# Kernel optimization log

Measured on AMD Instinct MI355X. Metric: run time of the kernel, lower is better.

The kernel has to match this reference:

```python
import jax, jax.numpy as jnp
import numpy as np

B, C, H, W = 4, 64, 64, 64
C8 = C // 8


def cl_attention(x, gamma):
    # DANet CAM-style channel attention: [B,C,H,W] -> [B,C,H,W]
    b, c, h, w = x.shape
    xf = x.reshape(b, c, h * w)                       # b c n
    energy = jnp.einsum('bcn,bdn->bcd', xf, xf)       # b c c
    energy = jnp.max(energy, axis=-1, keepdims=True) - energy
    attn = jax.nn.softmax(energy, axis=-1)
    out = jnp.einsum('bcd,bdn->bcn', attn, xf).reshape(b, c, h, w)
    return gamma * out + x


def setup_inputs() -> dict:
    key = jax.random.key(0)
    ks = jax.random.split(key, 8)
    s = 0.02
    return {
        'cnn_feat': jax.random.normal(ks[0], (B, C, H, W), jnp.float32),
        'vit_feat': jax.random.normal(ks[1], (B, C, H, W), jnp.float32),
        'Wq': jax.random.normal(ks[2], (C8, C), jnp.float32) * s,   # 1x1 conv kernel
        'bq': jnp.zeros((C8,), jnp.float32),
        'Wk': jax.random.normal(ks[3], (C8, C), jnp.float32) * s,
        'bk': jnp.zeros((C8,), jnp.float32),
        'Wv': jax.random.normal(ks[4], (C, C), jnp.float32) * s,
        'bv': jnp.zeros((C,), jnp.float32),
        'gamma': jnp.zeros((1,), jnp.float32),
        'gamma_cla_cnn': jnp.zeros((1,), jnp.float32),
        'gamma_cla_vit': jnp.zeros((1,), jnp.float32),
    }


def reference(cnn_feat, vit_feat, Wq, bq, Wk, bk, Wv, bv, gamma,
              gamma_cla_cnn, gamma_cla_vit):
    b, c, h, w = cnn_feat.shape
    n = h * w

    cnn_att = cl_attention(cnn_feat, gamma_cla_cnn)   # b c h w
    vit_att = cl_attention(vit_feat, gamma_cla_vit)   # b c h w

    # query: 1x1 conv -> view(b, C8, n) -> permute -> (b, n, C8)
    q = jnp.einsum('bchw,oc->bhwo', cnn_att, Wq).reshape(b, n, -1) + bq

    # vit: rearrange 'b c h w -> b (h w) c'
    vit_flat = vit_att.reshape(b, c, n).transpose(0, 2, 1)          # b n c
    k = vit_flat @ Wk.T + bk                                        # b n C8
    v = vit_flat @ Wv.T + bv                                        # b n C

    energy = jnp.einsum('bqd,bkd->bqk', q, k)                       # b n n
    attn = jax.nn.softmax(energy, axis=-1)
    out = jnp.einsum('bqk,bkc->bqc', attn, v)                       # b n c
    out = out.transpose(0, 2, 1).reshape(b, c, h, w)                # 'b (h w) c -> b c h w'
    return gamma * out + cnn_feat
```

## Files before the change

### kernel.cpp

```cpp
#include <hip/hip_runtime.h>
#include <hip/hip_bf16.h>

#define BSZ 4
#define CC 64
#define NN 4096
#define CN (CC*NN)
#define BCN (BSZ*CN)

typedef __attribute__((ext_vector_type(4))) float    f4v;
typedef __attribute__((ext_vector_type(4))) int      i4v;
typedef __attribute__((ext_vector_type(2))) int      i2v;
typedef __attribute__((ext_vector_type(8))) short    s8v;

__device__ __forceinline__ unsigned pack_bf16(float lo, float hi) {
    unsigned l = __builtin_bit_cast(unsigned, lo);
    unsigned h = __builtin_bit_cast(unsigned, hi);
    return (h & 0xFFFF0000u) | (l >> 16);
}
__device__ __forceinline__ unsigned pack2(float lo, float hi) {
    float2 f2; f2.x = lo; f2.y = hi;
    __hip_bfloat162 h = __float22bfloat162_rn(f2);
    unsigned u;
    __builtin_memcpy(&u, &h, 4);
    return u;
}

__global__ __launch_bounds__(256) void gram_k(const float* __restrict__ cnn,
                                              const float* __restrict__ vit,
                                              float* __restrict__ part) {
    __shared__ __align__(16) float sXT[128*68];
    int t = threadIdx.x;
    int blk = blockIdx.x;
    int ch = blk & 31, b = (blk >> 5) & 3, i2 = blk >> 7;
    const float* X = (i2 ? vit : cnn) + b * CN;
    int n0 = ch * 128;
#pragma unroll
    for (int j = 0; j < 8; j++) {
        int idx = t + j * 256;
        int c = idx >> 5, n4 = idx & 31;
        f4v val = *(const f4v*)&X[c * NN + n0 + n4 * 4];
        int base = (n4 * 4) * 68 + c;
        sXT[base]       = val[0];
        sXT[base + 68]  = val[1];
        sXT[base + 136] = val[2];
        sXT[base + 204] = val[3];
    }
    __syncthreads();
    int tc = (t & 15) * 4, td = (t >> 4) * 4;
    f4v acc[4];
#pragma unroll
    for (int i = 0; i < 4; i++) acc[i] = (f4v){0.f, 0.f, 0.f, 0.f};
#pragma unroll 4
    for (int k = 0; k < 128; k++) {
        f4v a  = *(const f4v*)&sXT[k * 68 + tc];
        f4v bb = *(const f4v*)&sXT[k * 68 + td];
#pragma unroll
        for (int i = 0; i < 4; i++) acc[i] += a[i] * bb;
    }
    float* dst = part + ch * 32768 + (i2 * 4 + b) * 4096;
#pragma unroll
    for (int i = 0; i < 4; i++) *(f4v*)&dst[(tc + i) * 64 + td] = acc[i];
}

__global__ void gred_k(const float* __restrict__ part, float* __restrict__ G) {
    int row = blockIdx.x;
    int d = threadIdx.x;
    float s = 0.f;
#pragma unroll 8
    for (int ch = 0; ch < 32; ch++) s += part[ch * 32768 + row * 64 + d];
    float mn = s;
#pragma unroll
    for (int off = 1; off < 64; off <<= 1) mn = fminf(mn, __shfl_xor(mn, off));
    float e = __expf(mn - s);
    float sm = e;
#pragma unroll
    for (int off = 1; off < 64; off <<= 1) sm += __shfl_xor(sm, off);
    G[row * 64 + d] = e / sm;
}

__global__ __launch_bounds__(256) void qkvw_k(const float* __restrict__ cnn,
                                              const float* __restrict__ vit,
                                              const float* __restrict__ G,
                                              const float* __restrict__ Wq,
                                              const float* __restrict__ Wk,
                                              const float* __restrict__ Wv,
                                              const float* __restrict__ gcnn,
                                              const float* __restrict__ gvit,
                                              const float* __restrict__ bq,
                                              const float* __restrict__ bk,
                                              const float* __restrict__ bv,
                                              ushort* __restrict__ qb,
                                              ushort* __restrict__ kb,
                                              ushort* __restrict__ vF) {
    __shared__ __align__(16) float sA[8192];
    __shared__ float sWt[5200];
    int t = threadIdx.x;
    int b = blockIdx.x >> 6, ktg = blockIdx.x & 63, n0 = ktg * 64;
    int w = t >> 6, lane = t & 63, c15 = lane & 15, q4 = lane >> 4;
    int n = n0 + w * 16 + c15;
    const float LOG2E = 1.44269504f;

#pragma unroll
    for (int i = 0; i < 4; i++) {
        int idx = (i * 256 + t) * 4;
        *(f4v*)&sA[idx]        = *(const f4v*)&G[(size_t)b * 4096 + idx];
        *(f4v*)&sA[4096 + idx] = *(const f4v*)&G[(size_t)(4 + b) * 4096 + idx];
    }
    __syncthreads();

    {
        int r16 = w, c = t & 63;
        float gc = *gcnn, gv = *gvit;
        float acc[4][5];
#pragma unroll
        for (int mi = 0; mi < 4; mi++)
#pragma unroll
            for (int tl = 0; tl < 5; tl++) acc[mi][tl] = 0.f;
#pragma unroll 4
        for (int d = 0; d < 64; d++) {
            float av = sA[4096 + d * 64 + c];
            float ac = sA[d * 64 + c];
#pragma unroll
            for (int mi = 0; mi < 4; mi++) {
                int m = mi * 4 + r16;
                if (mi < 2)
                    acc[mi][0] += Wq[m * 64 + d] * ac;
                else
                    acc[mi][0] += Wk[(m - 8) * 64 + d] * av;
#pragma unroll
                for (int tl = 1; tl < 5; tl++)
                    acc[mi][tl] += Wv[((tl - 1) * 16 + m) * 64 + d] * av;
            }
        }
#pragma unroll
        for (int mi = 0; mi < 4; mi++) {
            int m = mi * 4 + r16;
            if (mi < 2)
                sWt[m * 65 + c] = gc * acc[mi][0] + Wq[m * 64 + c];
            else
                sWt[m * 65 + c] = gv * acc[mi][0] + Wk[(m - 8) * 64 + c];
#pragma unroll
            for (int tl = 1; tl < 5; tl++)
                sWt[tl * 1040 + m * 65 + c] =
                    gv * acc[mi][tl] + Wv[((tl - 1) * 16 + m) * 64 + c];
        }
    }
    __syncthreads();

    s8v A[10];
#pragma unroll
    for (int i = 0; i < 10; i++) {
        int tile = i >> 1, frag = i & 1;
        const float* src = &sWt[tile * 1040 + (lane & 15) * 65 + frag * 32 + q4 * 8];
        i4v o;
#pragma unroll
        for (int p = 0; p < 4; p++)
            o[p] = (int)pack_bf16(src[2 * p], src[2 * p + 1]);
        A[i] = __builtin_bit_cast(s8v, o);
    }

    s8v Bc[2], Bv[2];
#pragma unroll
    for (int f = 0; f < 2; f++) {
        i4v pc, pv;
#pragma unroll
        for (int p = 0; p < 4; p++) {
            int c0 = f * 32 + q4 * 8 + p * 2;
            size_t a0 = (size_t)b * CN + (size_t)c0 * NN + n;
            pc[p] = (int)pack_bf16(cnn[a0], cnn[a0 + NN]);
            pv[p] = (int)pack_bf16(vit[a0], vit[a0 + NN]);
        }
        Bc[f] = __builtin_bit_cast(s8v, pc);
        Bv[f] = __builtin_bit_cast(s8v, pv);
    }

    f4v acc = *(const f4v*)(bq + (q4 & 1) * 4);
    acc = __builtin_amdgcn_mfma_f32_16x16x32_bf16(A[0], Bc[0], acc, 0, 0, 0);
    acc = __builtin_amdgcn_mfma_f32_16x16x32_bf16(A[1], Bc[1], acc, 0, 0, 0);
    if (q4 < 2) {
        unsigned d0 = pack_bf16(acc[0] * LOG2E, acc[1] * LOG2E);
        unsigned d1 = pack_bf16(acc[2] * LOG2E, acc[3] * LOG2E);
        unsigned long long v = ((unsigned long long)d1 << 32) | d0;
        *(unsigned long long*)&qb[(size_t)(b * NN + n) * 8 + q4 * 4] = v;
    }
    acc = *(const f4v*)(bk + (q4 & 1) * 4);
    acc = __builtin_amdgcn_mfma_f32_16x16x32_bf16(A[0], Bv[0], acc, 0, 0, 0);
    acc = __builtin_amdgcn_mfma_f32_16x16x32_bf16(A[1], Bv[1], acc, 0, 0, 0);
    if (q4 >= 2) {
        unsigned d0 = pack_bf16(acc[0], acc[1]), d1 = pack_bf16(acc[2], acc[3]);
        unsigned long long v = ((unsigned long long)d1 << 32) | d0;
        *(unsigned long long*)&kb[(size_t)(b * NN + n) * 8 + (q4 - 2) * 4] = v;
    }
    float* vbuf = sA;
#pragma unroll
    for (int tile = 1; tile < 5; tile++) {
        acc = *(const f4v*)(bv + (tile - 1) * 16 + q4 * 4);
        acc = __builtin_amdgcn_mfma_f32_16x16x32_bf16(A[tile * 2],     Bv[0], acc, 0, 0, 0);
        acc = __builtin_amdgcn_mfma_f32_16x16x32_bf16(A[tile * 2 + 1], Bv[1], acc, 0, 0, 0);
#pragma unroll
        for (int r = 0; r < 4; r++)
            vbuf[((tile - 1) * 16 + q4 * 4 + r) * 67 + w * 16 + c15] = acc[r];
    }
    __syncthreads();
    {
        int nt = w;
#pragma unroll
        for (int F = 0; F < 2; F++) {
            float vv[8];
#pragma unroll
            for (int e = 0; e < 8; e++)
                vv[e] = vbuf[(nt * 16 + c15) * 67 + 32 * F + 16 * (e >> 2)
                             + 4 * q4 + (e & 3)];
            i4v o;
#pragma unroll
            for (int p = 0; p < 4; p++)
                o[p] = (int)pack_bf16(vv[2 * p], vv[2 * p + 1]);
            *(i4v*)&vF[((size_t)((b * 64 + ktg) * 8 + nt * 2 + F)) * 512 + lane * 8] = o;
        }
    }
}

__global__ __launch_bounds__(256, 2) void flashB(
        const ushort* __restrict__ qb, const ushort* __restrict__ kb,
        const ushort* __restrict__ vF, const float* __restrict__ cnn,
        const float* __restrict__ gamma, float* __restrict__ out) {
    __shared__ __align__(16) float sO[2][64 * 68];
    __shared__ float sL[4][64];
    __shared__ float sRv[64];

    int t = threadIdx.x;
    int lane = t & 63, w = t >> 6;
    int c15 = lane & 15, q4 = lane >> 4;
    int blk = blockIdx.x;
    int b = blk >> 6, q0 = (blk & 63) * 64;
    float gm = *gamma;

    s8v qB[4];
#pragma unroll
    for (int g = 0; g < 4; g++) {
        i4v qa = (i4v){0, 0, 0, 0};
        if (q4 == 0)
            qa = *(const i4v*)(qb + (size_t)(b * NN + q0 + g * 16 + c15) * 8);
        qB[g] = __builtin_bit_cast(s8v, qa);
    }

    f4v accO[4][4];
#pragma unroll
    for (int g = 0; g < 4; g++)
#pragma unroll
        for (int nt = 0; nt < 4; nt++) accO[g][nt] = (f4v){0.f, 0.f, 0.f, 0.f};
    float lacc[4] = {0.f, 0.f, 0.f, 0.f};

    const ushort* kbb = kb + (size_t)b * NN * 8 + (size_t)c15 * 8;
    const ushort* vfb = vF + (size_t)b * 64 * 8 * 512 + (size_t)lane * 8;
    int kq = w * 1024;

    i4v bkc[4];
#pragma unroll
    for (int nt = 0; nt < 4; nt++)
        bkc[nt] = *(const i4v*)(kbb + (size_t)(kq + nt * 16) * 8);

    for (int kt = 0; kt < 16; kt++) {
        int ktg = (kq >> 6) + kt;
        i4v vA[2][4];
#pragma unroll
        for (int F = 0; F < 2; F++)
#pragma unroll
            for (int nt = 0; nt < 4; nt++)
                vA[F][nt] = *(const i4v*)(vfb +
                    (size_t)(ktg * 8 + nt * 2 + F) * 512);
        i4v bkn[4];
        if (kt < 15) {
#pragma unroll
            for (int nt = 0; nt < 4; nt++)
                bkn[nt] = *(const i4v*)(kbb +
                    (size_t)(kq + (kt + 1) * 64 + nt * 16) * 8);
        }

#pragma unroll
        for (int g = 0; g < 4; g++) {
            f4v z = (f4v){0.f, 0.f, 0.f, 0.f};
            f4v S[4];
#pragma unroll
            for (int nt = 0; nt < 4; nt++)
                S[nt] = __builtin_amdgcn_mfma_f32_16x16x32_bf16(
                    __builtin_bit_cast(s8v, bkc[nt]), qB[g], z, 0, 0, 0);
            f4v p[4];
            float ps = 0.f;
#pragma unroll
            for (int nt = 0; nt < 4; nt++)
#pragma unroll
                for (int rr = 0; rr < 4; rr++) {
                    p[nt][rr] = __builtin_amdgcn_exp2f(S[nt][rr]);
                    ps += p[nt][rr];
                }
            lacc[g] += ps;
            s8v Bp[2];
#pragma unroll
            for (int F = 0; F < 2; F++) {
                i4v bp;
                bp[0] = (int)pack2(p[2 * F][0],     p[2 * F][1]);
                bp[1] = (int)pack2(p[2 * F][2],     p[2 * F][3]);
                bp[2] = (int)pack2(p[2 * F + 1][0], p[2 * F + 1][1]);
                bp[3] = (int)pack2(p[2 * F + 1][2], p[2 * F + 1][3]);
                Bp[F] = __builtin_bit_cast(s8v, bp);
            }
            __builtin_amdgcn_s_setprio(1);
#pragma unroll
            for (int F = 0; F < 2; F++)
#pragma unroll
                for (int nt = 0; nt < 4; nt++)
                    accO[g][nt] = __builtin_amdgcn_mfma_f32_16x16x32_bf16(
                        __builtin_bit_cast(s8v, vA[F][nt]), Bp[F],
                        accO[g][nt], 0, 0, 0);
            __builtin_amdgcn_s_setprio(0);
        }
        if (kt < 15) {
#pragma unroll
            for (int nt = 0; nt < 4; nt++) bkc[nt] = bkn[nt];
        }
    }

#pragma unroll
    for (int g = 0; g < 4; g++) {
        lacc[g] += __shfl_xor(lacc[g], 16);
        lacc[g] += __shfl_xor(lacc[g], 32);
        if (q4 == 0) sL[w][g * 16 + c15] = lacc[g];
    }
    if (w >= 2) {
        float* s = sO[w - 2];
#pragma unroll
        for (int g = 0; g < 4; g++)
#pragma unroll
            for (int nt = 0; nt < 4; nt++)
#pragma unroll
                for (int rr = 0; rr < 4; rr++)
                    s[(nt * 16 + q4 * 4 + rr) * 68 + g * 16 + c15] = accO[g][nt][rr];
    }
    __syncthreads();
    if (w < 2) {
        float* s = sO[w];
#pragma unroll
        for (int g = 0; g < 4; g++)
#pragma unroll
            for (int nt = 0; nt < 4; nt++)
#pragma unroll
                for (int rr = 0; rr < 4; rr++)
                    accO[g][nt][rr] += s[(nt * 16 + q4 * 4 + rr) * 68 + g * 16 + c15];
    }
    if (w == 1) {
        float* s = sO[1];
#pragma unroll
        for (int g = 0; g < 4; g++)
#pragma unroll
            for (int nt = 0; nt < 4; nt++)
#pragma unroll
                for (int rr = 0; rr < 4; rr++)
                    s[(nt * 16 + q4 * 4 + rr) * 68 + g * 16 + c15] = accO[g][nt][rr];
    }
    if (w == 2) {
        float Ls = sL[0][lane] + sL[1][lane] + sL[2][lane] + sL[3][lane];
        sRv[lane] = gm / Ls;
    }
    __syncthreads();
    if (w == 0) {
        float* s1 = sO[1];
        float* s0 = sO[0];
#pragma unroll
        for (int g = 0; g < 4; g++)
#pragma unroll
            for (int nt = 0; nt < 4; nt++)
#pragma unroll
                for (int rr = 0; rr < 4; rr++) {
                    int off = (nt * 16 + q4 * 4 + rr) * 68 + g * 16 + c15;
                    s0[off] = accO[g][nt][rr] + s1[off];
                }
    }
    __syncthreads();
#pragma unroll
    for (int it = 0; it < 4; it++) {
        int c = it * 16 + (t >> 4), l16 = t & 15, q = l16 * 4;
        f4v o  = *(const f4v*)&sO[0][c * 68 + q];
        f4v rv = *(const f4v*)&sRv[q];
        size_t gi = (size_t)(b * 64 + c) * NN + q0 + q;
        f4v cv = *(const f4v*)&cnn[gi];
        *(f4v*)&out[gi] = o * rv + cv;
    }
}

extern "C" void kernel_launch(void* const* d_in, const int* in_sizes, int n_in,
                              void* d_out, int out_size, void* d_ws, size_t ws_size,
                              hipStream_t stream) {
    const float* cnn  = (const float*)d_in[0];
    const float* vit  = (const float*)d_in[1];
    const float* Wq   = (const float*)d_in[2];
    const float* bq   = (const float*)d_in[3];
    const float* Wk   = (const float*)d_in[4];
    const float* bk   = (const float*)d_in[5];
    const float* Wv   = (const float*)d_in[6];
    const float* bv   = (const float*)d_in[7];
    const float* gam  = (const float*)d_in[8];
    const float* gcnn = (const float*)d_in[9];
    const float* gvit = (const float*)d_in[10];
    float* out = (float*)d_out;

    float* ws = (float*)d_ws;
    float*  part = ws;
    float*  G    = ws + 1048576;
    ushort* qb   = (ushort*)(ws + 1081344);
    ushort* kb   = (ushort*)(ws + 1146880);
    ushort* vF   = (ushort*)(ws + 1212416);

    gram_k<<<256, 256, 0, stream>>>(cnn, vit, part);
    gred_k<<<512, 64,  0, stream>>>(part, G);
    qkvw_k<<<256, 256, 0, stream>>>(cnn, vit, G, Wq, Wk, Wv, gcnn, gvit,
                                    bq, bk, bv, qb, kb, vF);
    flashB<<<256, 256, 0, stream>>>(qb, kb, vF, cnn, gam, out);
}
```

Before: 123.0 us.

## Split flash attention keys across eight waves and coalesce gram partial layout

The flash kernel now runs 512 threads per block, so eight waves each handle 512 keys instead of four waves handling 1024. A tree reduction of the partial outputs through four shared-memory buffers replaces the old two-buffer scheme. The gram kernel stages its 64x64 partial tile through shared memory and writes it contiguously per chunk, and the reduction kernel reads it with vector loads and shuffles. The aim is more latency hiding and coalesced partial traffic, at the cost of more shared memory, extra barriers and possible occupancy limits at 512 threads.

Result: no change. 121.5 us (-1.2%).

```diff
diff --git a/kernel.cpp b/kernel.cpp
--- a/kernel.cpp
+++ b/kernel.cpp
@@ -57,25 +57,53 @@
 #pragma unroll
         for (int i = 0; i < 4; i++) acc[i] += a[i] * bb;
     }
-    float* dst = part + ch * 32768 + (i2 * 4 + b) * 4096;
-#pragma unroll
-    for (int i = 0; i < 4; i++) *(f4v*)&dst[(tc + i) * 64 + td] = acc[i];
+    __syncthreads();
+    float* sOut = sXT;
+#pragma unroll
+    for (int i = 0; i < 4; i++)
+        *(f4v*)&sOut[(tc + i) * 65 + td] = acc[i];
+    __syncthreads();
+    float* dst = part + (size_t)((i2 * 4 + b) * 32 + ch) * 4096;
+#pragma unroll
+    for (int j = 0; j < 4; j++) {
+        int flat = j * 1024 + t * 4;
+        int r = flat >> 6, d = flat & 63;
+        *(f4v*)&dst[flat] = *(const f4v*)&sOut[r * 65 + d];
+    }
 }
 
 __global__ void gred_k(const float* __restrict__ part, float* __restrict__ G) {
-    int row = blockIdx.x;
-    int d = threadIdx.x;
-    float s = 0.f;
-#pragma unroll 8
-    for (int ch = 0; ch < 32; ch++) s += part[ch * 32768 + row * 64 + d];
-    float mn = s;
-#pragma unroll
-    for (int off = 1; off < 64; off <<= 1) mn = fminf(mn, __shfl_xor(mn, off));
-    float e = __expf(mn - s);
-    float sm = e;
-#pragma unroll
-    for (int off = 1; off < 64; off <<= 1) sm += __shfl_xor(sm, off);
-    G[row * 64 + d] = e / sm;
+    int R = blockIdx.x;
+    int t = threadIdx.x;
+    int i2b = R >> 6, r = R & 63;
+    int l16 = t & 15, grp = t >> 4;
+    const float* base = part + (size_t)i2b * 32 * 4096 + r * 64 + l16 * 4;
+    f4v s = (f4v){0.f, 0.f, 0.f, 0.f};
+#pragma unroll
+    for (int c8 = 0; c8 < 8; c8++)
+        s += *(const f4v*)(base + (size_t)(c8 * 4 + grp) * 4096);
+#pragma unroll
+    for (int off = 16; off < 64; off <<= 1) {
+        s[0] += __shfl_xor(s[0], off);
+        s[1] += __shfl_xor(s[1], off);
+        s[2] += __shfl_xor(s[2], off);
+        s[3] += __shfl_xor(s[3], off);
+    }
+    float mn = fminf(fminf(s[0], s[1]), fminf(s[2], s[3]));
+#pragma unroll
+    for (int off = 1; off < 16; off <<= 1) mn = fminf(mn, __shfl_xor(mn, off));
+    f4v e;
+    float sm = 0.f;
+#pragma unroll
+    for (int j = 0; j < 4; j++) { e[j] = __expf(mn - s[j]); sm += e[j]; }
+#pragma unroll
+    for (int off = 1; off < 16; off <<= 1) sm += __shfl_xor(sm, off);
+    if (t < 16) {
+        f4v o;
+#pragma unroll
+        for (int j = 0; j < 4; j++) o[j] = e[j] / sm;
+        *(f4v*)&G[(size_t)R * 64 + l16 * 4] = o;
+    }
 }
 
 __global__ __launch_bounds__(256) void qkvw_k(const float* __restrict__ cnn,
@@ -220,13 +248,13 @@
     }
 }
 
-__global__ __launch_bounds__(256, 2) void flashB(
+__global__ __launch_bounds__(512, 2) void flashB(
         const ushort* __restrict__ qb, const ushort* __restrict__ kb,
         const ushort* __restrict__ vF, const float* __restrict__ cnn,
         const float* __restrict__ gamma, float* __restrict__ out) {
-    __shared__ __align__(16) float sO[2][64 * 68];
-    __shared__ float sL[4][64];
-    __shared__ float sRv[64];
+    __shared__ __align__(16) float sO[4][64 * 68];
+    __shared__ float sL[8][64];
+    __shared__ __align__(16) float sRv[64];
 
     int t = threadIdx.x;
     int lane = t & 63, w = t >> 6;
@@ -253,14 +281,14 @@
 
     const ushort* kbb = kb + (size_t)b * NN * 8 + (size_t)c15 * 8;
     const ushort* vfb = vF + (size_t)b * 64 * 8 * 512 + (size_t)lane * 8;
-    int kq = w * 1024;
+    int kq = w * 512;
 
     i4v bkc[4];
 #pragma unroll
     for (int nt = 0; nt < 4; nt++)
         bkc[nt] = *(const i4v*)(kbb + (size_t)(kq + nt * 16) * 8);
 
-    for (int kt = 0; kt < 16; kt++) {
+    for (int kt = 0; kt < 8; kt++) {
         int ktg = (kq >> 6) + kt;
         i4v vA[2][4];
 #pragma unroll
@@ -270,7 +298,7 @@
                 vA[F][nt] = *(const i4v*)(vfb +
                     (size_t)(ktg * 8 + nt * 2 + F) * 512);
         i4v bkn[4];
-        if (kt < 15) {
+        if (kt < 7) {
 #pragma unroll
             for (int nt = 0; nt < 4; nt++)
                 bkn[nt] = *(const i4v*)(kbb +
@@ -315,7 +343,7 @@
                         accO[g][nt], 0, 0, 0);
             __builtin_amdgcn_s_setprio(0);
         }
-        if (kt < 15) {
+        if (kt < 7) {
 #pragma unroll
             for (int nt = 0; nt < 4; nt++) bkc[nt] = bkn[nt];
         }
@@ -327,8 +355,8 @@
         lacc[g] += __shfl_xor(lacc[g], 32);
         if (q4 == 0) sL[w][g * 16 + c15] = lacc[g];
     }
-    if (w >= 2) {
-        float* s = sO[w - 2];
+
+    auto WRS = [&](float* s) {
 #pragma unroll
         for (int g = 0; g < 4; g++)
 #pragma unroll
@@ -336,10 +364,8 @@
 #pragma unroll
                 for (int rr = 0; rr < 4; rr++)
                     s[(nt * 16 + q4 * 4 + rr) * 68 + g * 16 + c15] = accO[g][nt][rr];
-    }
-    __syncthreads();
-    if (w < 2) {
-        float* s = sO[w];
+    };
+    auto ADS = [&](const float* s) {
 #pragma unroll
         for (int g = 0; g < 4; g++)
 #pragma unroll
@@ -347,44 +373,36 @@
 #pragma unroll
                 for (int rr = 0; rr < 4; rr++)
                     accO[g][nt][rr] += s[(nt * 16 + q4 * 4 + rr) * 68 + g * 16 + c15];
-    }
-    if (w == 1) {
-        float* s = sO[1];
-#pragma unroll
-        for (int g = 0; g < 4; g++)
-#pragma unroll
-            for (int nt = 0; nt < 4; nt++)
-#pragma unroll
-                for (int rr = 0; rr < 4; rr++)
-                    s[(nt * 16 + q4 * 4 + rr) * 68 + g * 16 + c15] = accO[g][nt][rr];
-    }
-    if (w == 2) {
-        float Ls = sL[0][lane] + sL[1][lane] + sL[2][lane] + sL[3][lane];
+    };
+
+    if (w >= 4) WRS(sO[w - 4]);
+    __syncthreads();
+    if (w < 4)  ADS(sO[w]);
+    if (w == 2 || w == 3) WRS(sO[w]);
+    if (w == 4) {
+        float Ls = 0.f;
+#pragma unroll
+        for (int i = 0; i < 8; i++) Ls += sL[i][lane];
         sRv[lane] = gm / Ls;
     }
     __syncthreads();
-    if (w == 0) {
-        float* s1 = sO[1];
-        float* s0 = sO[0];
-#pragma unroll
-        for (int g = 0; g < 4; g++)
-#pragma unroll
-            for (int nt = 0; nt < 4; nt++)
-#pragma unroll
-                for (int rr = 0; rr < 4; rr++) {
-                    int off = (nt * 16 + q4 * 4 + rr) * 68 + g * 16 + c15;
-                    s0[off] = accO[g][nt][rr] + s1[off];
-                }
-    }
-    __syncthreads();
-#pragma unroll
-    for (int it = 0; it < 4; it++) {
-        int c = it * 16 + (t >> 4), l16 = t & 15, q = l16 * 4;
-        f4v o  = *(const f4v*)&sO[0][c * 68 + q];
-        f4v rv = *(const f4v*)&sRv[q];
-        size_t gi = (size_t)(b * 64 + c) * NN + q0 + q;
-        f4v cv = *(const f4v*)&cnn[gi];
-        *(f4v*)&out[gi] = o * rv + cv;
+    if (w == 0) ADS(sO[2]);
+    if (w == 1) { ADS(sO[3]); WRS(sO[1]); }
+    __syncthreads();
+    if (w == 0) { ADS(sO[1]); WRS(sO[0]); }
+    __syncthreads();
+
+    {
+        int c = t >> 3, qo = (t & 7) * 8;
+        f4v o0 = *(const f4v*)&sO[0][c * 68 + qo];
+        f4v o1 = *(const f4v*)&sO[0][c * 68 + qo + 4];
+        f4v r0 = *(const f4v*)&sRv[qo];
+        f4v r1 = *(const f4v*)&sRv[qo + 4];
+        size_t gi = (size_t)(b * 64 + c) * NN + q0 + qo;
+        f4v c0 = *(const f4v*)&cnn[gi];
+        f4v c1 = *(const f4v*)&cnn[gi + 4];
+        *(f4v*)&out[gi]     = o0 * r0 + c0;
+        *(f4v*)&out[gi + 4] = o1 * r1 + c1;
     }
 }
 
@@ -415,5 +433,5 @@
     gred_k<<<512, 64,  0, stream>>>(part, G);
     qkvw_k<<<256, 256, 0, stream>>>(cnn, vit, G, Wq, Wk, Wv, gcnn, gvit,
                                     bq, bk, bv, qb, kb, vF);
-    flashB<<<256, 256, 0, stream>>>(qb, kb, vF, cnn, gam, out);
-}
+    flashB<<<256, 512, 0, stream>>>(qb, kb, vF, cnn, gam, out);
+}
```
